# Kernel tuning notes

Hardware: AMD Instinct MI355X
Metric: run time of the kernel (lower is better)

## Reference

```python
import jax, jax.numpy as jnp
import numpy as np

BINS = 64
MIN_VAL, MAX_VAL = 0.0, 1.0


def soft_histogram(x, bins=BINS, min_val=MIN_VAL, max_val=MAX_VAL):
    # x: (B, C, H, W)
    B, C, H, W = x.shape
    x_flat = x.reshape(B, C, -1)                       # (B, C, HW)
    bin_width = (max_val - min_val) / bins
    centers = jnp.linspace(min_val + bin_width / 2, max_val - bin_width / 2, bins,
                           dtype=x.dtype)              # (bins,)
    sigma = bin_width
    # broadcasted Gaussian kernel weights, reduced over pixels -> (B, C, bins)
    diff = x_flat[..., None] - centers                 # (B, C, HW, bins)
    weights = jnp.exp(-(diff ** 2) / (2.0 * sigma ** 2))
    hist = weights.sum(axis=2)                         # (B, C, bins)
    hist = hist / (hist.sum(axis=-1, keepdims=True) + 1e-8)
    return hist


def setup_inputs() -> dict:
    key = jax.random.key(0)
    k1, k2 = jax.random.split(key)
    pred = jax.random.uniform(k1, (4, 3, 256, 256), dtype=jnp.float32)
    target = jax.random.uniform(k2, (4, 3, 256, 256), dtype=jnp.float32)
    return {"pred": pred, "target": target}


def reference(pred, target):
    pred_hist = soft_histogram(pred, BINS)
    target_hist = soft_histogram(target, BINS)
    pred_cdf = jnp.cumsum(pred_hist, axis=-1)
    target_cdf = jnp.cumsum(target_hist, axis=-1)
    return jnp.mean(jnp.abs(pred_cdf - target_cdf))
```

## Files before the change

kernel.cpp:

```cpp
#include <hip/hip_runtime.h>
#include <hip/hip_bf16.h>


#define BINS 64
#define NCH 12
#define HW 65536
#define BPC 32
#define PIX_PER_BLOCK (HW / BPC)
#define THREADS 256
#define PIX_PER_THREAD (PIX_PER_BLOCK / THREADS)

__device__ __forceinline__ float fast_exp2(float x) {
#if __has_builtin(__builtin_amdgcn_exp2f)
    return __builtin_amdgcn_exp2f(x);
#else
    return exp2f(x);
#endif
}

__global__ void zero_ws(float* ws, int n) {
    int i = blockIdx.x * blockDim.x + threadIdx.x;
    if (i < n) ws[i] = 0.0f;
}

__global__ __launch_bounds__(THREADS) void hist_kernel(
        const float* __restrict__ pred,
        const float* __restrict__ target,
        float* __restrict__ hist) {
    const int blk   = blockIdx.x;
    const int ch    = blk / BPC;
    const int chunk = blk % BPC;
    const float* src = (ch < NCH) ? (pred + (size_t)ch * HW)
                                  : (target + (size_t)(ch - NCH) * HW);
    const int base = chunk * PIX_PER_BLOCK + threadIdx.x;

    const float S  = 0.84932180028801904f;
    const float XS = 64.0f * S;

    float acc[BINS];
    #pragma unroll
    for (int j = 0; j < BINS; ++j) acc[j] = 0.0f;

    for (int p = 0; p < PIX_PER_THREAD; ++p) {
        float x  = src[base + p * THREADS];
        float xs = x * XS;
        #pragma unroll
        for (int j = 0; j < BINS; ++j) {
            float u = xs - (j + 0.5f) * S;
            acc[j] += fast_exp2(-(u * u));
        }
    }

    const int lane = threadIdx.x & 63;
    #pragma unroll
    for (int k = 32; k >= 1; k >>= 1) {
        const bool hi = (lane & k) != 0;
        #pragma unroll
        for (int i = 0; i < k; ++i) {
            float keepv = hi ? acc[i + k] : acc[i];
            float sendv = hi ? acc[i] : acc[i + k];
            acc[i] = keepv + __shfl_xor(sendv, k, 64);
        }
    }
    float wave_sum = acc[0];

    __shared__ float bh[BINS];
    if (threadIdx.x < BINS) bh[threadIdx.x] = 0.0f;
    __syncthreads();
    atomicAdd(&bh[lane], wave_sum);
    __syncthreads();
    if (threadIdx.x < BINS)
        atomicAdd(&hist[ch * BINS + threadIdx.x], bh[threadIdx.x]);
}

__global__ __launch_bounds__(NCH * 64) void final_kernel(
        const float* __restrict__ hist, float* __restrict__ out) {
    const int w    = threadIdx.x >> 6;
    const int lane = threadIdx.x & 63;

    float ph = hist[w * BINS + lane];
    float th = hist[(NCH + w) * BINS + lane];

    float ps = ph, ts = th;
    #pragma unroll
    for (int d = 1; d < 64; d <<= 1) {
        float a = __shfl_up(ps, d, 64);
        float b = __shfl_up(ts, d, 64);
        if (lane >= d) { ps += a; ts += b; }
    }
    float ptot = __shfl(ps, 63, 64);
    float ttot = __shfl(ts, 63, 64);
    float pc = ps / (ptot + 1e-8f);
    float tc = ts / (ttot + 1e-8f);
    float dv = fabsf(pc - tc);

    #pragma unroll
    for (int k = 32; k >= 1; k >>= 1) dv += __shfl_xor(dv, k, 64);

    __shared__ float warr[NCH];
    if (lane == 0) warr[w] = dv;
    __syncthreads();
    if (threadIdx.x == 0) {
        float s = 0.0f;
        #pragma unroll
        for (int i = 0; i < NCH; ++i) s += warr[i];
        out[0] = s / (float)(NCH * BINS);
    }
}

extern "C" void kernel_launch(void* const* d_in, const int* in_sizes, int n_in,
                              void* d_out, int out_size, void* d_ws, size_t ws_size,
                              hipStream_t stream) {
    const float* pred   = (const float*)d_in[0];
    const float* target = (const float*)d_in[1];
    float* hist = (float*)d_ws;
    float* out  = (float*)d_out;

    zero_ws<<<dim3((2 * NCH * BINS + 255) / 256), dim3(256), 0, stream>>>(
        hist, 2 * NCH * BINS);
    hist_kernel<<<dim3(2 * NCH * BPC), dim3(THREADS), 0, stream>>>(
        pred, target, hist);
    final_kernel<<<dim3(1), dim3(NCH * 64), 0, stream>>>(hist, out);
}
```

Baseline: 78.67 us.

## Truncate Gaussian to a 17-bin window with shared-memory atomic scatter

Replaces the dense 64-bin exp evaluation per pixel with a window of ±8 bins around the nearest center. The window weights come from a constant Gaussian table multiplied by a geometric exp factor, so each pixel needs two exp2 calls instead of 64. The weights are scattered with per-wave shared-memory atomics into padded histograms. Pixels are loaded as float4. The intent is to remove most transcendental work and the large register accumulator and shuffle reduction, at the cost of LDS atomic contention and truncating tails below about 1e-14.

```diff
diff --git a/kernel.cpp b/kernel.cpp
--- a/kernel.cpp
+++ b/kernel.cpp
@@ -1,5 +1,4 @@
 #include <hip/hip_runtime.h>
-#include <hip/hip_bf16.h>
 
 
 #define BINS 64
@@ -8,7 +7,10 @@
 #define BPC 32
 #define PIX_PER_BLOCK (HW / BPC)
 #define THREADS 256
-#define PIX_PER_THREAD (PIX_PER_BLOCK / THREADS)
+#define R 8
+#define WIN (2 * R + 1)
+#define PADBINS (BINS + 2 * R)
+#define NWAVES (THREADS / 64)
 
 __device__ __forceinline__ float fast_exp2(float x) {
 #if __has_builtin(__builtin_amdgcn_exp2f)
@@ -27,50 +29,58 @@
         const float* __restrict__ pred,
         const float* __restrict__ target,
         float* __restrict__ hist) {
+    constexpr float CK[WIN] = {
+        1.2664165549094176e-14f, 2.2897348456455526e-11f, 1.5229979744712628e-08f,
+        3.7266531720786709e-06f, 3.3546262790251185e-04f, 1.1108996538242306e-02f,
+        1.3533528323661270e-01f, 6.0653065971263342e-01f, 1.0f,
+        6.0653065971263342e-01f, 1.3533528323661270e-01f, 1.1108996538242306e-02f,
+        3.3546262790251185e-04f, 3.7266531720786709e-06f, 1.5229979744712628e-08f,
+        2.2897348456455526e-11f, 1.2664165549094176e-14f };
+
     const int blk   = blockIdx.x;
     const int ch    = blk / BPC;
     const int chunk = blk % BPC;
     const float* src = (ch < NCH) ? (pred + (size_t)ch * HW)
                                   : (target + (size_t)(ch - NCH) * HW);
-    const int base = chunk * PIX_PER_BLOCK + threadIdx.x;
 
-    const float S  = 0.84932180028801904f;
-    const float XS = 64.0f * S;
+    __shared__ float h[NWAVES][PADBINS];
+    for (int t = threadIdx.x; t < NWAVES * PADBINS; t += THREADS)
+        (&h[0][0])[t] = 0.0f;
+    __syncthreads();
 
-    float acc[BINS];
+    float* hw_ = h[threadIdx.x >> 6];
+
+    const float4* src4 = (const float4*)(src + chunk * PIX_PER_BLOCK);
+    float4 a = src4[threadIdx.x];
+    float4 b = src4[threadIdx.x + THREADS];
+    float px[8] = {a.x, a.y, a.z, a.w, b.x, b.y, b.z, b.w};
+
+    const float L = 1.4426950408889634f;
+
     #pragma unroll
-    for (int j = 0; j < BINS; ++j) acc[j] = 0.0f;
-
-    for (int p = 0; p < PIX_PER_THREAD; ++p) {
-        float x  = src[base + p * THREADS];
-        float xs = x * XS;
+    for (int p = 0; p < 8; ++p) {
+        float xt = px[p] * 64.0f - 0.5f;
+        float fi = rintf(xt);
+        fi = fminf(fmaxf(fi, 0.0f), 63.0f);
+        float f  = xt - fi;
+        int   i  = (int)fi;
+        float P  = fast_exp2(-(0.5f * L) * (f * f + (float)(2 * R) * f));
+        float B  = fast_exp2(L * f);
+        float* hp = hw_ + i;
         #pragma unroll
-        for (int j = 0; j < BINS; ++j) {
-            float u = xs - (j + 0.5f) * S;
-            acc[j] += fast_exp2(-(u * u));
+        for (int t = 0; t < WIN; ++t) {
+            atomicAdd(&hp[t], CK[t] * P);
+            P *= B;
         }
     }
 
-    const int lane = threadIdx.x & 63;
-    #pragma unroll
-    for (int k = 32; k >= 1; k >>= 1) {
-        const bool hi = (lane & k) != 0;
+    __syncthreads();
+    if (threadIdx.x < BINS) {
+        float s = 0.0f;
         #pragma unroll
-        for (int i = 0; i < k; ++i) {
-            float keepv = hi ? acc[i + k] : acc[i];
-            float sendv = hi ? acc[i] : acc[i + k];
-            acc[i] = keepv + __shfl_xor(sendv, k, 64);
-        }
+        for (int c = 0; c < NWAVES; ++c) s += h[c][R + threadIdx.x];
+        atomicAdd(&hist[ch * BINS + threadIdx.x], s);
     }
-    float wave_sum = acc[0];
-
-    __shared__ float bh[BINS];
-    if (threadIdx.x < BINS) bh[threadIdx.x] = 0.0f;
-    __syncthreads();
-    atomicAdd(&bh[lane], wave_sum);
-    __syncthreads();
-    if (threadIdx.x < BINS)
-        atomicAdd(&hist[ch * BINS + threadIdx.x], bh[threadIdx.x]);
 }
 
 __global__ __launch_bounds__(NCH * 64) void final_kernel(
```

Result: slower. 192.3 us (+144.4%).
